# Performance work log

Hardware: AMD Instinct MI355X
Metric: run time of the kernel (lower is better)

The kernel has to match this reference:

```python
import jax, jax.numpy as jnp
import numpy as np

N = 4096
IN = 64          # input_size
QD = 16          # query_vector_dim
CI = 2 * IN + 1  # 129, MLP_Param input dim


def _xavier(key, shape):
    fan_in, fan_out = shape[-2], shape[-1]
    bound = float(np.sqrt(6.0 / (fan_in + fan_out)))
    return jax.random.uniform(key, shape, jnp.float32, -bound, bound)


def setup_inputs() -> dict:
    key = jax.random.key(0)
    ks = jax.random.split(key, 10)
    return {
        "x": jax.random.normal(ks[0], (N, IN + 1), jnp.float32),
        "h": jax.random.normal(ks[1], (N, IN), jnp.float32),
        "query_vectors": jax.random.normal(ks[2], (N, QD), jnp.float32),
        "adj": jax.random.uniform(ks[3], (N, N), jnp.float32),
        "nodes_ind": jnp.arange(N, dtype=jnp.int64 if jax.config.jax_enable_x64 else jnp.int32),
        "W_r": _xavier(ks[4], (QD, CI, IN)),
        "b_r": _xavier(ks[5], (QD, IN)),
        "W_u": _xavier(ks[6], (QD, CI, IN)),
        "b_u": _xavier(ks[7], (QD, IN)),
        "W_c": _xavier(ks[8], (QD, CI, IN)),
        "b_c": _xavier(ks[9], (QD, IN)),
    }


def _mlp_param(xv, q, W, b):
    # per-node dynamic weights: [n, CI, IN]
    Wn = jnp.einsum('nd,dio->nio', q, W)
    return jnp.einsum('ni,nio->no', xv, Wn) + q @ b


def reference(x, h, query_vectors, adj, nodes_ind, W_r, b_r, W_u, b_u, W_c, b_c):
    combined = adj @ jnp.concatenate([x, h], axis=-1)          # [N, 129]
    cg = combined[nodes_ind]                                    # [M, 129]
    r = jax.nn.sigmoid(_mlp_param(cg, query_vectors, W_r, b_r))
    u = jax.nn.sigmoid(_mlp_param(cg, query_vectors, W_u, b_u))
    h2 = h.at[nodes_ind].set(r * h[nodes_ind])                  # h[nodes_ind] = r*h[nodes_ind]
    combined_new = jnp.concatenate([x, h2], axis=-1)[nodes_ind]  # no adj mixing second time
    cand = jnp.tanh(_mlp_param(combined_new, query_vectors, W_c, b_c))
    return (1.0 - u) * h2[nodes_ind] + u * cand
```

## Files before the change

### kernel.cpp

```cpp
#include <hip/hip_runtime.h>
#include <math.h>


#define NN   4096
#define XCC  65
#define HCC  64
#define QDIM 16
#define CI   129
#define CST  132
#define AKST 520
#define XVST 148
#define GSTRIDE 147456

typedef unsigned short u16;
typedef __attribute__((ext_vector_type(4))) unsigned short ushort4_t;
typedef __attribute__((ext_vector_type(8))) unsigned short ushort8_t;
typedef __attribute__((ext_vector_type(8))) short bf16x8;
typedef __attribute__((ext_vector_type(16))) float f32x16;

__device__ __forceinline__ void split2(float a, u16& hi, u16& lo) {
  unsigned u = __float_as_uint(a);
  hi = (u16)(u >> 16);
  float rec = __uint_as_float(u & 0xFFFF0000u);
  float lf = a - rec;
  unsigned v = __float_as_uint(lf);
  v += 0x7FFF + ((v >> 16) & 1);
  lo = (u16)(v >> 16);
}

__device__ __forceinline__ void gload_lds16(const void* gsrc, void* ldst) {
  __builtin_amdgcn_global_load_lds(
      (const __attribute__((address_space(1))) unsigned int*)gsrc,
      (__attribute__((address_space(3))) unsigned int*)ldst, 16, 0, 0);
}

__global__ __launch_bounds__(256) void k0_pack(const float* __restrict__ x,
                                               const float* __restrict__ h,
                                               u16* __restrict__ Bh,
                                               u16* __restrict__ Bl,
                                               const float* __restrict__ Wr,
                                               const float* __restrict__ Wu,
                                               const float* __restrict__ Wc,
                                               u16* __restrict__ Wh,
                                               u16* __restrict__ Wl) {
  __shared__ float sT[64][161];
  const int t = threadIdx.x;
  if (blockIdx.x < 64) {
    const int n0 = blockIdx.x * 64;
    for (int f = t; f < 64 * XCC; f += 256) {
      int n = f / XCC, c = f - n * XCC;
      sT[n][c] = x[(size_t)(n0 + n) * XCC + c];
    }
    for (int f = t; f < 64 * HCC; f += 256) {
      int n = f >> 6, c = f & 63;
      sT[n][XCC + c] = h[(size_t)(n0 + n) * HCC + c];
    }
    for (int f = t; f < 64 * 31; f += 256) {
      int n = f / 31, c = f - n * 31;
      sT[n][CI + c] = 0.f;
    }
    __syncthreads();
    for (int idx = t; idx < 5 * 4 * 64; idx += 256) {
      const int lane = idx & 63;
      const int ksl = (idx >> 6) & 3;
      const int ct = idx >> 8;
      const int nl = ksl * 16 + (lane >> 5) * 8;
      const int feat = ct * 32 + (lane & 31);
      ushort8_t vh, vl;
#pragma unroll
      for (int j = 0; j < 8; ++j) {
        u16 hi, lo; split2(sT[nl + j][feat], hi, lo);
        vh[j] = hi; vl[j] = lo;
      }
      const size_t off = (((size_t)ct * 256 + (blockIdx.x * 4) + ksl) * 64 + lane) * 8;
      *(ushort8_t*)(Bh + off) = vh;
      *(ushort8_t*)(Bl + off) = vl;
    }
  } else {
    int gid = (blockIdx.x - 64) * 256 + t;
    if (gid >= 3 * 16 * 2 * 9 * 64) return;
    int lane = gid & 63;
    int rest = gid >> 6;
    int kst = rest % 9; rest /= 9;
    int ct = rest & 1; rest >>= 1;
    int d = rest & 15; rest >>= 4;
    const float* W = (rest == 0) ? Wr : (rest == 1 ? Wu : Wc);
    const int o = ct * 32 + (lane & 31);
    const int i0 = kst * 16 + (lane >> 5) * 8;
    ushort8_t vh, vl;
#pragma unroll
    for (int j = 0; j < 8; ++j) {
      int i = i0 + j;
      float v = (i < CI) ? W[((size_t)d * CI + i) * 64 + o] : 0.f;
      u16 hi, lo; split2(v, hi, lo);
      vh[j] = hi; vl[j] = lo;
    }
    const size_t off = (size_t)gid * 8;
    *(ushort8_t*)(Wh + off) = vh;
    *(ushort8_t*)(Wl + off) = vl;
  }
}

template <int SPKT>
__global__ __launch_bounds__(256, 4) void k1_mfma(const float* __restrict__ adj,
                                                  const u16* __restrict__ Bh,
                                                  const u16* __restrict__ Bl,
                                                  float* __restrict__ P1) {
  constexpr int KLEN = 4096 / SPKT;
  constexpr int STEPS = KLEN / 16;
  __shared__ u16 sAh[2][2][64][8];
  __shared__ u16 sAl[2][2][64][8];
  __shared__ u16 sB[3][10][512];
  __shared__ u16 sScratch[512];
  const int t = threadIdx.x;
  const int lane = t & 63;
  const int w = t >> 6;
  const int rgrp = w & 1;
  const int cthalf = w >> 1;
  const int m0 = blockIdx.x * 64;
  const int sp = blockIdx.y;
  const int ct0 = cthalf ? 3 : 0;
  const int R = t >> 2;
  const int ksts = t & 3;
  const int srg = R >> 5, srl = R & 31;
  const int skh = ksts >> 1, sj0 = (ksts & 1) * 4;

  f32x16 a0, a1, a2;
#pragma unroll
  for (int r = 0; r < 16; ++r) { a0[r] = 0.f; a1[r] = 0.f; a2[r] = 0.f; }

  const float* aptr = adj + (size_t)(m0 + R) * NN + sp * KLEN + ksts * 4;
  float4 va, vb, vc;

#define LOADA(it, tgt) tgt = *(const float4*)(aptr + (it) * 16);

#define CONV4(src, abuf)                                                       \
  {                                                                            \
    u16 h0, h1, h2, h3, l0, l1, l2, l3;                                        \
    split2(src.x, h0, l0); split2(src.y, h1, l1);                              \
    split2(src.z, h2, l2); split2(src.w, h3, l3);                              \
    ushort4_t hv = {h0, h1, h2, h3};                                           \
    ushort4_t lv = {l0, l1, l2, l3};                                           \
    *(ushort4_t*)&sAh[abuf][srg][srl + 32 * skh][sj0] = hv;                    \
    *(ushort4_t*)&sAl[abuf][srg][srl + 32 * skh][sj0] = lv;                    \
  }

#define BDMA(it, bbuf)                                                         \
  {                                                                            \
    _Pragma("unroll")                                                          \
    for (int j = 0; j < 3; ++j) {                                              \
      const int c = w + 4 * j;                                                 \
      const int ct = (c < 10) ? (c >> 1) : 0;                                  \
      const int hl = (c < 10) ? (c & 1) : 0;                                   \
      const int ks = sp * STEPS + (it);                                        \
      const u16* src =                                                         \
          (hl ? Bl : Bh) + (((size_t)ct * 256 + ks) * 64 + lane) * 8;          \
      gload_lds16(src, (c < 10) ? &sB[bbuf][c][0] : &sScratch[0]);             \
    }                                                                          \
  }

#define BAR(N)                                                                 \
  asm volatile("s_waitcnt vmcnt(" #N ") lgkmcnt(0)" ::: "memory");             \
  __builtin_amdgcn_sched_barrier(0);                                           \
  __builtin_amdgcn_s_barrier();                                                \
  __builtin_amdgcn_sched_barrier(0);

#define COMPUTE(abuf, bbuf)                                                    \
  {                                                                            \
    bf16x8 ah = *(const bf16x8*)&sAh[abuf][rgrp][lane][0];                     \
    bf16x8 al = *(const bf16x8*)&sAl[abuf][rgrp][lane][0];                     \
    const int cb = ct0 * 2;                                                    \
    bf16x8 b0h = *(const bf16x8*)&sB[bbuf][cb + 0][lane * 8];                  \
    bf16x8 b0l = *(const bf16x8*)&sB[bbuf][cb + 1][lane * 8];                  \
    bf16x8 b1h = *(const bf16x8*)&sB[bbuf][cb + 2][lane * 8];                  \
    bf16x8 b1l = *(const bf16x8*)&sB[bbuf][cb + 3][lane * 8];                  \
    a0 = __builtin_amdgcn_mfma_f32_32x32x16_bf16(ah, b0h, a0, 0, 0, 0);        \
    a1 = __builtin_amdgcn_mfma_f32_32x32x16_bf16(ah, b1h, a1, 0, 0, 0);        \
    a0 = __builtin_amdgcn_mfma_f32_32x32x16_bf16(al, b0h, a0, 0, 0, 0);        \
    a1 = __builtin_amdgcn_mfma_f32_32x32x16_bf16(al, b1h, a1, 0, 0, 0);        \
    a0 = __builtin_amdgcn_mfma_f32_32x32x16_bf16(ah, b0l, a0, 0, 0, 0);        \
    a1 = __builtin_amdgcn_mfma_f32_32x32x16_bf16(ah, b1l, a1, 0, 0, 0);        \
    if (cthalf == 0) {                                                         \
      bf16x8 b2h = *(const bf16x8*)&sB[bbuf][cb + 4][lane * 8];                \
      bf16x8 b2l = *(const bf16x8*)&sB[bbuf][cb + 5][lane * 8];                \
      a2 = __builtin_amdgcn_mfma_f32_32x32x16_bf16(ah, b2h, a2, 0, 0, 0);      \
      a2 = __builtin_amdgcn_mfma_f32_32x32x16_bf16(al, b2h, a2, 0, 0, 0);      \
      a2 = __builtin_amdgcn_mfma_f32_32x32x16_bf16(ah, b2l, a2, 0, 0, 0);      \
    }                                                                          \
  }

  LOADA(0, va);
  BDMA(0, 0);
  LOADA(1, vb);
  BDMA(1, 1);
  LOADA(2, vc);
  CONV4(va, 0);
  BAR(5)
#pragma unroll
  for (int it = 0; it < STEPS; ++it) {
    const int abuf = it & 1;
    const int bbuf = it % 3;
    if (it < STEPS - 2) BDMA(it + 2, (it + 2) % 3);
    if (it <= STEPS - 4) {
      if ((it % 3) == 0) { LOADA(it + 3, va); }
      else if ((it % 3) == 1) { LOADA(it + 3, vb); }
      else { LOADA(it + 3, vc); }
    }
    COMPUTE(abuf, bbuf);
    if (it < STEPS - 1) {
      if (((it + 1) % 3) == 0) { CONV4(va, abuf ^ 1); }
      else if (((it + 1) % 3) == 1) { CONV4(vb, abuf ^ 1); }
      else { CONV4(vc, abuf ^ 1); }
    }
    if (it <= STEPS - 4) { BAR(5) }
    else if (it == STEPS - 3) { BAR(4) }
    else if (it == STEPS - 2) { BAR(0) }
  }
#undef LOADA
#undef CONV4
#undef BDMA
#undef BAR
#undef COMPUTE
  float* outp = P1 + (size_t)sp * NN * CST;
  const int colb = lane & 31;
  const int rbase = m0 + rgrp * 32 + 4 * (lane >> 5);
  {
    const int colg = ct0 * 32 + colb;
#pragma unroll
    for (int r = 0; r < 16; ++r)
      outp[(size_t)(rbase + (r & 3) + 8 * (r >> 2)) * CST + colg] = a0[r];
  }
  {
    const int colg = (ct0 + 1) * 32 + colb;
    if (colg < CST) {
#pragma unroll
      for (int r = 0; r < 16; ++r)
        outp[(size_t)(rbase + (r & 3) + 8 * (r >> 2)) * CST + colg] = a1[r];
    }
  }
  if (cthalf == 0) {
    const int colg = 64 + colb;
#pragma unroll
    for (int r = 0; r < 16; ++r)
      outp[(size_t)(rbase + (r & 3) + 8 * (r >> 2)) * CST + colg] = a2[r];
  }
}

#define PACKA()                                                                \
  for (int s = t; s < 9 * 64; s += 512) {                                      \
    int kst = s >> 6, l = s & 63;                                              \
    int row = l & 31, k0i = kst * 16 + (l >> 5) * 8;                           \
    ushort8_t vh, vl;                                                          \
    _Pragma("unroll")                                                          \
    for (int j = 0; j < 8; ++j) {                                              \
      u16 hi, lo; split2(sXV[row][k0i + j], hi, lo);                           \
      vh[j] = hi; vl[j] = lo;                                                  \
    }                                                                          \
    *(ushort8_t*)&sAh[kst * AKST + l * 8] = vh;                                \
    *(ushort8_t*)&sAl[kst * AKST + l * 8] = vl;                                \
  }

template <int SPKT>
__global__ __launch_bounds__(512, 2) void k2_gate(
    const float* __restrict__ P1, const float* __restrict__ h,
    const float* __restrict__ q, const u16* __restrict__ Wh,
    const u16* __restrict__ Wl, const float* __restrict__ br,
    const float* __restrict__ bu, float* __restrict__ U,
    float* __restrict__ H2) {
  __shared__ float sXV[32][XVST];
  __shared__ u16 sAh[9 * AKST], sAl[9 * AKST];
  __shared__ float sQ[32][16];
  __shared__ float sX0[8][16][64];
  __shared__ float sX1[8][16][64];
  const int t = threadIdx.x;
  const int n0 = blockIdx.x * 32;
  const int g = blockIdx.y;
  for (int f = t; f < 32 * 33; f += 512) {
    int n = f / 33, c4 = f - n * 33;
    const float* p = P1 + (size_t)(n0 + n) * CST + c4 * 4;
    float sx = 0.f, sy = 0.f, sz = 0.f, sw = 0.f;
#pragma unroll
    for (int sp = 0; sp < SPKT; ++sp) {
      float4 v = *(const float4*)(p + (size_t)sp * NN * CST);
      sx += v.x; sy += v.y; sz += v.z; sw += v.w;
    }
    sXV[n][c4 * 4 + 0] = sx; sXV[n][c4 * 4 + 1] = sy;
    sXV[n][c4 * 4 + 2] = sz; sXV[n][c4 * 4 + 3] = sw;
  }
  for (int f = t; f < 32 * 3; f += 512) {
    float4 z = {0, 0, 0, 0};
    *(float4*)&sXV[f / 3][132 + (f % 3) * 4] = z;
  }
  sQ[t >> 4][t & 15] = q[(size_t)(n0 + (t >> 4)) * QDIM + (t & 15)];
  __syncthreads();
  PACKA();
  __syncthreads();
  const int lane = t & 63, dh = t >> 6;
  const u16* gh = Wh + (size_t)g * GSTRIDE;
  const u16* gl = Wl + (size_t)g * GSTRIDE;

  f32x16 aC0, aC1;
#pragma unroll
  for (int r = 0; r < 16; ++r) { aC0[r] = 0.f; aC1[r] = 0.f; }
#pragma unroll
  for (int dd = 0; dd < 2; ++dd) {
    const int d = dh * 2 + dd;
    const size_t b0 = (((size_t)d * 2 + 0) * 576 + lane) * 8;
    const size_t b1 = (((size_t)d * 2 + 1) * 576 + lane) * 8;
    f32x16 t00, t01, t02, t10, t11, t12;
#pragma unroll
    for (int r = 0; r < 16; ++r) {
      t00[r] = 0.f; t01[r] = 0.f; t02[r] = 0.f;
      t10[r] = 0.f; t11[r] = 0.f; t12[r] = 0.f;
    }
#pragma unroll
    for (int kst = 0; kst < 9; ++kst) {
      bf16x8 ah = *(const bf16x8*)&sAh[kst * AKST + lane * 8];
      bf16x8 al = *(const bf16x8*)&sAl[kst * AKST + lane * 8];
      bf16x8 b0h = *(const bf16x8*)(gh + b0 + kst * 512);
      bf16x8 b0l = *(const bf16x8*)(gl + b0 + kst * 512);
      bf16x8 b1h = *(const bf16x8*)(gh + b1 + kst * 512);
      bf16x8 b1l = *(const bf16x8*)(gl + b1 + kst * 512);
      t00 = __builtin_amdgcn_mfma_f32_32x32x16_bf16(ah, b0h, t00, 0, 0, 0);
      t10 = __builtin_amdgcn_mfma_f32_32x32x16_bf16(ah, b1h, t10, 0, 0, 0);
      t01 = __builtin_amdgcn_mfma_f32_32x32x16_bf16(al, b0h, t01, 0, 0, 0);
      t11 = __builtin_amdgcn_mfma_f32_32x32x16_bf16(al, b1h, t11, 0, 0, 0);
      t02 = __builtin_amdgcn_mfma_f32_32x32x16_bf16(ah, b0l, t02, 0, 0, 0);
      t12 = __builtin_amdgcn_mfma_f32_32x32x16_bf16(ah, b1l, t12, 0, 0, 0);
    }
#pragma unroll
    for (int r = 0; r < 16; ++r) {
      int node = (r & 3) + 8 * (r >> 2) + 4 * (lane >> 5);
      float qd = sQ[node][d];
      aC0[r] += qd * (t00[r] + t01[r] + t02[r]);
      aC1[r] += qd * (t10[r] + t11[r] + t12[r]);
    }
  }
#pragma unroll
  for (int r = 0; r < 16; ++r) {
    sX0[dh][r][lane] = aC0[r];
    sX1[dh][r][lane] = aC1[r];
  }
  __syncthreads();
  const float* bias = g ? bu : br;
  const int col0 = lane & 31, col1 = 32 + col0;
#pragma unroll
  for (int i = 0; i < 2; ++i) {
    const int rr = dh * 2 + i;
    const int node = (rr & 3) + 8 * (rr >> 2) + 4 * (lane >> 5);
    float s0 = 0.f, s1 = 0.f;
#pragma unroll
    for (int wv = 0; wv < 8; ++wv) {
      s0 += sX0[wv][rr][lane];
      s1 += sX1[wv][rr][lane];
    }
#pragma unroll
    for (int d = 0; d < 16; ++d) {
      float qd = sQ[node][d];
      s0 += qd * bias[(size_t)d * 64 + col0];
      s1 += qd * bias[(size_t)d * 64 + col1];
    }
    float sg0 = 1.f / (1.f + expf(-s0));
    float sg1 = 1.f / (1.f + expf(-s1));
    const int g0 = (n0 + node) * 64 + col0;
    const int g1 = (n0 + node) * 64 + col1;
    if (g == 0) {
      H2[g0] = sg0 * h[g0];
      H2[g1] = sg1 * h[g1];
    } else {
      U[g0] = sg0;
      U[g1] = sg1;
    }
  }
}

__global__ __launch_bounds__(512, 2) void k3_cand(
    const float* __restrict__ x, const float* __restrict__ H2,
    const float* __restrict__ q, const u16* __restrict__ Wh,
    const u16* __restrict__ Wl, const float* __restrict__ bc,
    const float* __restrict__ U, float* __restrict__ out) {
  __shared__ float sXV[32][XVST];
  __shared__ u16 sAh[9 * AKST], sAl[9 * AKST];
  __shared__ float sQ[32][16];
  __shared__ float sX0[8][16][64];
  const int t = threadIdx.x;
  const int n0 = blockIdx.x * 32;
  const int cto = blockIdx.y;
  for (int f = t; f < 32 * 144; f += 512) {
    int n = f / 144, i = f - n * 144;
    float v = 0.f;
    if (i < XCC) v = x[(size_t)(n0 + n) * XCC + i];
    else if (i < CI) v = H2[(size_t)(n0 + n) * HCC + (i - XCC)];
    sXV[n][i] = v;
  }
  sQ[t >> 4][t & 15] = q[(size_t)(n0 + (t >> 4)) * QDIM + (t & 15)];
  __syncthreads();
  PACKA();
  __syncthreads();
  const int lane = t & 63, dh = t >> 6;
  const u16* gh = Wh + (size_t)2 * GSTRIDE;
  const u16* gl = Wl + (size_t)2 * GSTRIDE;
  f32x16 acc;
#pragma unroll
  for (int r = 0; r < 16; ++r) acc[r] = 0.f;
#pragma unroll
  for (int dd = 0; dd < 2; ++dd) {
    const int d = dh * 2 + dd;
    const size_t bb = (((size_t)d * 2 + cto) * 576 + lane) * 8;
    f32x16 t0, t1, t2;
#pragma unroll
    for (int r = 0; r < 16; ++r) { t0[r] = 0.f; t1[r] = 0.f; t2[r] = 0.f; }
#pragma unroll
    for (int kst = 0; kst < 9; ++kst) {
      bf16x8 ah = *(const bf16x8*)&sAh[kst * AKST + lane * 8];
      bf16x8 al = *(const bf16x8*)&sAl[kst * AKST + lane * 8];
      bf16x8 bh = *(const bf16x8*)(gh + bb + kst * 512);
      bf16x8 bl = *(const bf16x8*)(gl + bb + kst * 512);
      t0 = __builtin_amdgcn_mfma_f32_32x32x16_bf16(ah, bh, t0, 0, 0, 0);
      t1 = __builtin_amdgcn_mfma_f32_32x32x16_bf16(al, bh, t1, 0, 0, 0);
      t2 = __builtin_amdgcn_mfma_f32_32x32x16_bf16(ah, bl, t2, 0, 0, 0);
    }
#pragma unroll
    for (int r = 0; r < 16; ++r) {
      int node = (r & 3) + 8 * (r >> 2) + 4 * (lane >> 5);
      acc[r] += sQ[node][d] * (t0[r] + t1[r] + t2[r]);
    }
  }
#pragma unroll
  for (int r = 0; r < 16; ++r) sX0[dh][r][lane] = acc[r];
  __syncthreads();
  const int colu = cto * 32 + (lane & 31);
#pragma unroll
  for (int i = 0; i < 2; ++i) {
    const int rr = dh * 2 + i;
    const int node = (rr & 3) + 8 * (rr >> 2) + 4 * (lane >> 5);
    float s = 0.f;
#pragma unroll
    for (int wv = 0; wv < 8; ++wv) s += sX0[wv][rr][lane];
#pragma unroll
    for (int d = 0; d < 16; ++d) s += sQ[node][d] * bc[(size_t)d * 64 + colu];
    float cand = tanhf(s);
    const int gidx = (n0 + node) * 64 + colu;
    float u = U[gidx], h2 = H2[gidx];
    out[gidx] = (1.f - u) * h2 + u * cand;
  }
}

extern "C" void kernel_launch(void* const* d_in, const int* in_sizes, int n_in,
                              void* d_out, int out_size, void* d_ws, size_t ws_size,
                              hipStream_t stream) {
  const float* x   = (const float*)d_in[0];
  const float* h   = (const float*)d_in[1];
  const float* q   = (const float*)d_in[2];
  const float* adj = (const float*)d_in[3];
  const float* Wr  = (const float*)d_in[5];
  const float* br  = (const float*)d_in[6];
  const float* Wu  = (const float*)d_in[7];
  const float* bu  = (const float*)d_in[8];
  const float* Wc  = (const float*)d_in[9];
  const float* bc  = (const float*)d_in[10];
  float* out = (float*)d_out;

  const size_t NEED16 = (size_t)16 * NN * CST * 4 + 2621440 + 1769472 + 2097152;
  const int spk = (ws_size >= NEED16) ? 16 : 8;

  char* ws = (char*)d_ws;
  const size_t OFF_P1 = 0;
  const size_t OFF_BP = OFF_P1 + (size_t)spk * NN * CST * 4;
  const size_t OFF_WH = OFF_BP + (size_t)2 * 5 * 256 * 64 * 8 * 2;
  const size_t OFF_WL = OFF_WH + (size_t)3 * GSTRIDE * 2;
  const size_t OFF_U  = OFF_WL + (size_t)3 * GSTRIDE * 2;
  const size_t OFF_H2 = OFF_U + (size_t)NN * HCC * 4;
  float* P1 = (float*)(ws + OFF_P1);
  u16*   Bh = (u16*)(ws + OFF_BP);
  u16*   Bl = (u16*)(ws + OFF_BP + (size_t)5 * 256 * 64 * 8 * 2);
  u16*   Wh = (u16*)(ws + OFF_WH);
  u16*   Wl = (u16*)(ws + OFF_WL);
  float* U  = (float*)(ws + OFF_U);
  float* H2 = (float*)(ws + OFF_H2);

  hipLaunchKernelGGL(k0_pack, dim3(280), dim3(256), 0, stream,
                     x, h, Bh, Bl, Wr, Wu, Wc, Wh, Wl);
  if (spk == 16) {
    hipLaunchKernelGGL(k1_mfma<16>, dim3(64, 16), dim3(256), 0, stream,
                       adj, Bh, Bl, P1);
    hipLaunchKernelGGL(k2_gate<16>, dim3(128, 2), dim3(512), 0, stream,
                       P1, h, q, Wh, Wl, br, bu, U, H2);
  } else {
    hipLaunchKernelGGL(k1_mfma<8>, dim3(64, 8), dim3(256), 0, stream,
                       adj, Bh, Bl, P1);
    hipLaunchKernelGGL(k2_gate<8>, dim3(128, 2), dim3(512), 0, stream,
                       P1, h, q, Wh, Wl, br, bu, U, H2);
  }
  hipLaunchKernelGGL(k3_cand, dim3(128, 2), dim3(512), 0, stream,
                     x, H2, q, Wh, Wl, bc, U, out);
}
```

Baseline: 75.78 us.

## Fuse gate and candidate kernels into one cooperative kernel with grid sync

```diff
diff --git a/kernel.cpp b/kernel.cpp
--- a/kernel.cpp
+++ b/kernel.cpp
@@ -1,4 +1,5 @@
 #include <hip/hip_runtime.h>
+#include <hip/hip_cooperative_groups.h>
 #include <math.h>
 
 
@@ -261,12 +262,13 @@
   }
 
 template <int SPKT>
-__global__ __launch_bounds__(512, 2) void k2_gate(
-    const float* __restrict__ P1, const float* __restrict__ h,
-    const float* __restrict__ q, const u16* __restrict__ Wh,
-    const u16* __restrict__ Wl, const float* __restrict__ br,
-    const float* __restrict__ bu, float* __restrict__ U,
-    float* __restrict__ H2) {
+__global__ __launch_bounds__(512, 2) void k23_coop(
+    const float* __restrict__ P1, const float* __restrict__ x,
+    const float* __restrict__ h, const float* __restrict__ q,
+    const u16* __restrict__ Wh, const u16* __restrict__ Wl,
+    const float* __restrict__ br, const float* __restrict__ bu,
+    const float* __restrict__ bc, float* __restrict__ H2,
+    float* __restrict__ out) {
   __shared__ float sXV[32][XVST];
   __shared__ u16 sAh[9 * AKST], sAl[9 * AKST];
   __shared__ float sQ[32][16];
@@ -274,7 +276,7 @@
   __shared__ float sX1[8][16][64];
   const int t = threadIdx.x;
   const int n0 = blockIdx.x * 32;
-  const int g = blockIdx.y;
+  const int cto = blockIdx.y;
   for (int f = t; f < 32 * 33; f += 512) {
     int n = f / 33, c4 = f - n * 33;
     const float* p = P1 + (size_t)(n0 + n) * CST + c4 * 4;
@@ -295,18 +297,23 @@
   __syncthreads();
   PACKA();
   __syncthreads();
+  for (int f = t; f < 32 * 65; f += 512) {
+    int n = f / 65, i = f - n * 65;
+    sXV[n][i] = x[(size_t)(n0 + n) * XCC + i];
+  }
   const int lane = t & 63, dh = t >> 6;
-  const u16* gh = Wh + (size_t)g * GSTRIDE;
-  const u16* gl = Wl + (size_t)g * GSTRIDE;
-
-  f32x16 aC0, aC1;
-#pragma unroll
-  for (int r = 0; r < 16; ++r) { aC0[r] = 0.f; aC1[r] = 0.f; }
+
+  f32x16 aR, aU;
+#pragma unroll
+  for (int r = 0; r < 16; ++r) { aR[r] = 0.f; aU[r] = 0.f; }
 #pragma unroll
   for (int dd = 0; dd < 2; ++dd) {
     const int d = dh * 2 + dd;
-    const size_t b0 = (((size_t)d * 2 + 0) * 576 + lane) * 8;
-    const size_t b1 = (((size_t)d * 2 + 1) * 576 + lane) * 8;
+    const size_t bb = (((size_t)d * 2 + cto) * 576 + lane) * 8;
+    const u16* rh = Wh + bb;
+    const u16* rl = Wl + bb;
+    const u16* uh = Wh + GSTRIDE + bb;
+    const u16* ul = Wl + GSTRIDE + bb;
     f32x16 t00, t01, t02, t10, t11, t12;
 #pragma unroll
     for (int r = 0; r < 16; ++r) {
@@ -317,10 +324,10 @@
     for (int kst = 0; kst < 9; ++kst) {
       bf16x8 ah = *(const bf16x8*)&sAh[kst * AKST + lane * 8];
       bf16x8 al = *(const bf16x8*)&sAl[kst * AKST + lane * 8];
-      bf16x8 b0h = *(const bf16x8*)(gh + b0 + kst * 512);
-      bf16x8 b0l = *(const bf16x8*)(gl + b0 + kst * 512);
-      bf16x8 b1h = *(const bf16x8*)(gh + b1 + kst * 512);
-      bf16x8 b1l = *(const bf16x8*)(gl + b1 + kst * 512);
+      bf16x8 b0h = *(const bf16x8*)(rh + kst * 512);
+      bf16x8 b0l = *(const bf16x8*)(rl + kst * 512);
+      bf16x8 b1h = *(const bf16x8*)(uh + kst * 512);
+      bf16x8 b1l = *(const bf16x8*)(ul + kst * 512);
       t00 = __builtin_amdgcn_mfma_f32_32x32x16_bf16(ah, b0h, t00, 0, 0, 0);
       t10 = __builtin_amdgcn_mfma_f32_32x32x16_bf16(ah, b1h, t10, 0, 0, 0);
       t01 = __builtin_amdgcn_mfma_f32_32x32x16_bf16(al, b0h, t01, 0, 0, 0);
@@ -332,104 +339,85 @@
     for (int r = 0; r < 16; ++r) {
       int node = (r & 3) + 8 * (r >> 2) + 4 * (lane >> 5);
       float qd = sQ[node][d];
-      aC0[r] += qd * (t00[r] + t01[r] + t02[r]);
-      aC1[r] += qd * (t10[r] + t11[r] + t12[r]);
+      aR[r] += qd * (t00[r] + t01[r] + t02[r]);
+      aU[r] += qd * (t10[r] + t11[r] + t12[r]);
     }
   }
 #pragma unroll
   for (int r = 0; r < 16; ++r) {
-    sX0[dh][r][lane] = aC0[r];
-    sX1[dh][r][lane] = aC1[r];
-  }
-  __syncthreads();
-  const float* bias = g ? bu : br;
-  const int col0 = lane & 31, col1 = 32 + col0;
+    sX0[dh][r][lane] = aR[r];
+    sX1[dh][r][lane] = aU[r];
+  }
+  __syncthreads();
+  const int colo = cto * 32 + (lane & 31);
+  float uval[2], h2own[2];
 #pragma unroll
   for (int i = 0; i < 2; ++i) {
     const int rr = dh * 2 + i;
     const int node = (rr & 3) + 8 * (rr >> 2) + 4 * (lane >> 5);
-    float s0 = 0.f, s1 = 0.f;
+    float sr = 0.f, su = 0.f;
 #pragma unroll
     for (int wv = 0; wv < 8; ++wv) {
-      s0 += sX0[wv][rr][lane];
-      s1 += sX1[wv][rr][lane];
+      sr += sX0[wv][rr][lane];
+      su += sX1[wv][rr][lane];
     }
 #pragma unroll
     for (int d = 0; d < 16; ++d) {
       float qd = sQ[node][d];
-      s0 += qd * bias[(size_t)d * 64 + col0];
-      s1 += qd * bias[(size_t)d * 64 + col1];
-    }
-    float sg0 = 1.f / (1.f + expf(-s0));
-    float sg1 = 1.f / (1.f + expf(-s1));
-    const int g0 = (n0 + node) * 64 + col0;
-    const int g1 = (n0 + node) * 64 + col1;
-    if (g == 0) {
-      H2[g0] = sg0 * h[g0];
-      H2[g1] = sg1 * h[g1];
-    } else {
-      U[g0] = sg0;
-      U[g1] = sg1;
-    }
-  }
-}
-
-__global__ __launch_bounds__(512, 2) void k3_cand(
-    const float* __restrict__ x, const float* __restrict__ H2,
-    const float* __restrict__ q, const u16* __restrict__ Wh,
-    const u16* __restrict__ Wl, const float* __restrict__ bc,
-    const float* __restrict__ U, float* __restrict__ out) {
-  __shared__ float sXV[32][XVST];
-  __shared__ u16 sAh[9 * AKST], sAl[9 * AKST];
-  __shared__ float sQ[32][16];
-  __shared__ float sX0[8][16][64];
-  const int t = threadIdx.x;
-  const int n0 = blockIdx.x * 32;
-  const int cto = blockIdx.y;
-  for (int f = t; f < 32 * 144; f += 512) {
-    int n = f / 144, i = f - n * 144;
-    float v = 0.f;
-    if (i < XCC) v = x[(size_t)(n0 + n) * XCC + i];
-    else if (i < CI) v = H2[(size_t)(n0 + n) * HCC + (i - XCC)];
-    sXV[n][i] = v;
-  }
-  sQ[t >> 4][t & 15] = q[(size_t)(n0 + (t >> 4)) * QDIM + (t & 15)];
+      sr += qd * br[(size_t)d * 64 + colo];
+      su += qd * bu[(size_t)d * 64 + colo];
+    }
+    float rg = 1.f / (1.f + expf(-sr));
+    uval[i] = 1.f / (1.f + expf(-su));
+    const int gidx = (n0 + node) * 64 + colo;
+    float h2v = rg * h[gidx];
+    h2own[i] = h2v;
+    sXV[node][XCC + colo] = h2v;
+    H2[gidx] = h2v;
+  }
+  cooperative_groups::this_grid().sync();
+
+  const int coto = cto ^ 1;
+  for (int f = t; f < 32 * 32; f += 512) {
+    int n = f >> 5, c = f & 31;
+    sXV[n][XCC + coto * 32 + c] = H2[(size_t)(n0 + n) * HCC + coto * 32 + c];
+  }
   __syncthreads();
   PACKA();
   __syncthreads();
-  const int lane = t & 63, dh = t >> 6;
-  const u16* gh = Wh + (size_t)2 * GSTRIDE;
-  const u16* gl = Wl + (size_t)2 * GSTRIDE;
-  f32x16 acc;
-#pragma unroll
-  for (int r = 0; r < 16; ++r) acc[r] = 0.f;
-#pragma unroll
-  for (int dd = 0; dd < 2; ++dd) {
-    const int d = dh * 2 + dd;
-    const size_t bb = (((size_t)d * 2 + cto) * 576 + lane) * 8;
-    f32x16 t0, t1, t2;
-#pragma unroll
-    for (int r = 0; r < 16; ++r) { t0[r] = 0.f; t1[r] = 0.f; t2[r] = 0.f; }
-#pragma unroll
-    for (int kst = 0; kst < 9; ++kst) {
-      bf16x8 ah = *(const bf16x8*)&sAh[kst * AKST + lane * 8];
-      bf16x8 al = *(const bf16x8*)&sAl[kst * AKST + lane * 8];
-      bf16x8 bh = *(const bf16x8*)(gh + bb + kst * 512);
-      bf16x8 bl = *(const bf16x8*)(gl + bb + kst * 512);
-      t0 = __builtin_amdgcn_mfma_f32_32x32x16_bf16(ah, bh, t0, 0, 0, 0);
-      t1 = __builtin_amdgcn_mfma_f32_32x32x16_bf16(al, bh, t1, 0, 0, 0);
-      t2 = __builtin_amdgcn_mfma_f32_32x32x16_bf16(ah, bl, t2, 0, 0, 0);
-    }
-#pragma unroll
-    for (int r = 0; r < 16; ++r) {
-      int node = (r & 3) + 8 * (r >> 2) + 4 * (lane >> 5);
-      acc[r] += sQ[node][d] * (t0[r] + t1[r] + t2[r]);
-    }
-  }
-#pragma unroll
-  for (int r = 0; r < 16; ++r) sX0[dh][r][lane] = acc[r];
-  __syncthreads();
-  const int colu = cto * 32 + (lane & 31);
+  {
+    const u16* gh = Wh + (size_t)2 * GSTRIDE;
+    const u16* gl = Wl + (size_t)2 * GSTRIDE;
+    f32x16 acc;
+#pragma unroll
+    for (int r = 0; r < 16; ++r) acc[r] = 0.f;
+#pragma unroll
+    for (int dd = 0; dd < 2; ++dd) {
+      const int d = dh * 2 + dd;
+      const size_t bb = (((size_t)d * 2 + cto) * 576 + lane) * 8;
+      f32x16 t0, t1, t2;
+#pragma unroll
+      for (int r = 0; r < 16; ++r) { t0[r] = 0.f; t1[r] = 0.f; t2[r] = 0.f; }
+#pragma unroll
+      for (int kst = 0; kst < 9; ++kst) {
+        bf16x8 ah = *(const bf16x8*)&sAh[kst * AKST + lane * 8];
+        bf16x8 al = *(const bf16x8*)&sAl[kst * AKST + lane * 8];
+        bf16x8 bh = *(const bf16x8*)(gh + bb + kst * 512);
+        bf16x8 bl = *(const bf16x8*)(gl + bb + kst * 512);
+        t0 = __builtin_amdgcn_mfma_f32_32x32x16_bf16(ah, bh, t0, 0, 0, 0);
+        t1 = __builtin_amdgcn_mfma_f32_32x32x16_bf16(al, bh, t1, 0, 0, 0);
+        t2 = __builtin_amdgcn_mfma_f32_32x32x16_bf16(ah, bl, t2, 0, 0, 0);
+      }
+#pragma unroll
+      for (int r = 0; r < 16; ++r) {
+        int node = (r & 3) + 8 * (r >> 2) + 4 * (lane >> 5);
+        acc[r] += sQ[node][d] * (t0[r] + t1[r] + t2[r]);
+      }
+    }
+#pragma unroll
+    for (int r = 0; r < 16; ++r) sX0[dh][r][lane] = acc[r];
+  }
+  __syncthreads();
 #pragma unroll
   for (int i = 0; i < 2; ++i) {
     const int rr = dh * 2 + i;
@@ -438,11 +426,10 @@
 #pragma unroll
     for (int wv = 0; wv < 8; ++wv) s += sX0[wv][rr][lane];
 #pragma unroll
-    for (int d = 0; d < 16; ++d) s += sQ[node][d] * bc[(size_t)d * 64 + colu];
+    for (int d = 0; d < 16; ++d) s += sQ[node][d] * bc[(size_t)d * 64 + colo];
     float cand = tanhf(s);
-    const int gidx = (n0 + node) * 64 + colu;
-    float u = U[gidx], h2 = H2[gidx];
-    out[gidx] = (1.f - u) * h2 + u * cand;
+    out[(size_t)(n0 + node) * HCC + colo] =
+        (1.f - uval[i]) * h2own[i] + uval[i] * cand;
   }
 }
 
@@ -461,7 +448,7 @@
   const float* bc  = (const float*)d_in[10];
   float* out = (float*)d_out;
 
-  const size_t NEED16 = (size_t)16 * NN * CST * 4 + 2621440 + 1769472 + 2097152;
+  const size_t NEED16 = (size_t)16 * NN * CST * 4 + 2621440 + 1769472 + 1048576;
   const int spk = (ws_size >= NEED16) ? 16 : 8;
 
   char* ws = (char*)d_ws;
@@ -469,29 +456,29 @@
   const size_t OFF_BP = OFF_P1 + (size_t)spk * NN * CST * 4;
   const size_t OFF_WH = OFF_BP + (size_t)2 * 5 * 256 * 64 * 8 * 2;
   const size_t OFF_WL = OFF_WH + (size_t)3 * GSTRIDE * 2;
-  const size_t OFF_U  = OFF_WL + (size_t)3 * GSTRIDE * 2;
-  const size_t OFF_H2 = OFF_U + (size_t)NN * HCC * 4;
-  float* P1 = (float*)(ws + OFF_P1);
+  const size_t OFF_H2 = OFF_WL + (size_t)3 * GSTRIDE * 2;
+  const float* P1 = (const float*)(ws + OFF_P1);
   u16*   Bh = (u16*)(ws + OFF_BP);
   u16*   Bl = (u16*)(ws + OFF_BP + (size_t)5 * 256 * 64 * 8 * 2);
-  u16*   Wh = (u16*)(ws + OFF_WH);
-  u16*   Wl = (u16*)(ws + OFF_WL);
-  float* U  = (float*)(ws + OFF_U);
+  const u16* Wh = (const u16*)(ws + OFF_WH);
+  const u16* Wl = (const u16*)(ws + OFF_WL);
   float* H2 = (float*)(ws + OFF_H2);
 
   hipLaunchKernelGGL(k0_pack, dim3(280), dim3(256), 0, stream,
-                     x, h, Bh, Bl, Wr, Wu, Wc, Wh, Wl);
+                     x, h, Bh, Bl, Wr, Wu, Wc, (u16*)Wh, (u16*)Wl);
+
+  void* args[] = {(void*)&P1, (void*)&x, (void*)&h, (void*)&q,
+                  (void*)&Wh, (void*)&Wl, (void*)&br, (void*)&bu,
+                  (void*)&bc, (void*)&H2, (void*)&out};
   if (spk == 16) {
     hipLaunchKernelGGL(k1_mfma<16>, dim3(64, 16), dim3(256), 0, stream,
-                       adj, Bh, Bl, P1);
-    hipLaunchKernelGGL(k2_gate<16>, dim3(128, 2), dim3(512), 0, stream,
-                       P1, h, q, Wh, Wl, br, bu, U, H2);
+                       adj, Bh, Bl, (float*)P1);
+    hipLaunchCooperativeKernel(k23_coop<16>, dim3(128, 2), dim3(512),
+                               args, 0u, stream);
   } else {
     hipLaunchKernelGGL(k1_mfma<8>, dim3(64, 8), dim3(256), 0, stream,
-                       adj, Bh, Bl, P1);
-    hipLaunchKernelGGL(k2_gate<8>, dim3(128, 2), dim3(512), 0, stream,
-                       P1, h, q, Wh, Wl, br, bu, U, H2);
-  }
-  hipLaunchKernelGGL(k3_cand, dim3(128, 2), dim3(512), 0, stream,
-                     x, H2, q, Wh, Wl, bc, U, out);
-}
+                       adj, Bh, Bl, (float*)P1);
+    hipLaunchCooperativeKernel(k23_coop<8>, dim3(128, 2), dim3(512),
+                               args, 0u, stream);
+  }
+}
```

Result: slower. 99.86 us (+31.8%).
